# Performance work log

Hardware: AMD Instinct MI355X
Metric: run time of the kernel (lower is better)

The kernel has to match this reference:

```python
import jax, jax.numpy as jnp
import numpy as np

DIM = 1024
N_HEADS = 16
HEAD_DIM = DIM // N_HEADS
SCALE = HEAD_DIM ** (-0.5)


def setup_inputs() -> dict:
    key = jax.random.key(0)
    ks = jax.random.split(key, 5)
    B, N = 2, 2048
    x = jax.random.normal(ks[0], (B, N, DIM), dtype=jnp.float32)
    # torch nn.Linear weight layout: (out_features, in_features)
    qkv_w = jax.random.normal(ks[1], (3 * DIM, DIM), dtype=jnp.float32) * 0.02
    qkv_b = jax.random.normal(ks[2], (3 * DIM,), dtype=jnp.float32) * 0.02
    proj_w = jax.random.normal(ks[3], (DIM, DIM), dtype=jnp.float32) * 0.02
    proj_b = jax.random.normal(ks[4], (DIM,), dtype=jnp.float32) * 0.02
    return {"x": x, "qkv_w": qkv_w, "qkv_b": qkv_b, "proj_w": proj_w, "proj_b": proj_b}


def reference(x, qkv_w, qkv_b, proj_w, proj_b):
    B, N, C = x.shape
    # QKV projection: (B,N,C) -> (B,N,3C)
    qkv = jnp.einsum('bnc,oc->bno', x, qkv_w) + qkv_b
    # (B,N,3,H,Dh) -> (3,B,H,N,Dh)
    qkv = qkv.reshape(B, N, 3, N_HEADS, HEAD_DIM).transpose(2, 0, 3, 1, 4)
    q, k, v = qkv[0], qkv[1], qkv[2]
    attn = jnp.einsum('bhqd,bhkd->bhqk', q, k) * SCALE
    attn = jax.nn.softmax(attn, axis=-1)
    out = jnp.einsum('bhqk,bhkd->bhqd', attn, v)
    out = out.transpose(0, 2, 1, 3).reshape(B, N, C)  # concat heads
    out = jnp.einsum('bnc,oc->bno', out, proj_w) + proj_b
    return out
```

## Files before the change

### kernel.cpp

```cpp
#include <hip/hip_runtime.h>

#define DIM 1024
#define NHEADS 16
#define HD 64
#define NSEQ 2048
#define MROWS 4096
#define QKV_LD 3072

typedef __attribute__((ext_vector_type(8))) short short8;
typedef __attribute__((ext_vector_type(4))) short short4v;
typedef __attribute__((ext_vector_type(4))) float f32x4;

typedef __attribute__((address_space(1))) void gvoid_t;
typedef __attribute__((address_space(3))) void lvoid_t;

#if __has_builtin(__builtin_amdgcn_exp2f)
#define EXP2(x) __builtin_amdgcn_exp2f(x)
#else
#define EXP2(x) exp2f(x)
#endif

#define EXP_SCALE 0.18033688011112042f

#define PHI(r) (((r) & 7) ^ ((((r) >> 3) & 3) << 1))

__device__ __forceinline__ unsigned short f2bf(float f) {
  unsigned int u = __builtin_bit_cast(unsigned int, f);
  u += 0x7FFFu + ((u >> 16) & 1u);
  return (unsigned short)(u >> 16);
}

__device__ __forceinline__ void gl_lds16(const void* g, void* l) {
  __builtin_amdgcn_global_load_lds((gvoid_t*)g, (lvoid_t*)l, 16, 0, 0);
}

__global__ __launch_bounds__(256) void cast_bf16_3(
    const float* __restrict__ x, const float* __restrict__ wq,
    const float* __restrict__ wp,
    unsigned short* __restrict__ xb, unsigned short* __restrict__ wqb,
    unsigned short* __restrict__ wpb)
{
  int g = blockIdx.x * 256 + threadIdx.x;
  const float* src;
  unsigned short* dst;
  if (g < 1048576)            { src = x  + (size_t)g * 4;              dst = xb  + (size_t)g * 4; }
  else if (g < 1048576 + 786432) { int t = g - 1048576; src = wq + (size_t)t * 4; dst = wqb + (size_t)t * 4; }
  else                        { int t = g - 1048576 - 786432; src = wp + (size_t)t * 4; dst = wpb + (size_t)t * 4; }
  float4 v = *(const float4*)src;
  ushort4 o;
  o.x = f2bf(v.x); o.y = f2bf(v.y); o.z = f2bf(v.z); o.w = f2bf(v.w);
  *(ushort4*)dst = o;
}

__global__ __launch_bounds__(256) void gemm_nt(
    const unsigned short* __restrict__ A,
    const unsigned short* __restrict__ Bw,
    const float* __restrict__ bias,
    int K, int mode,
    unsigned short* __restrict__ oq,
    unsigned short* __restrict__ ovt,
    float* __restrict__ of)
{
  __shared__ unsigned short As[128 * 64];
  __shared__ unsigned short Bs[128 * 64];

  const int tid  = threadIdx.x;
  const int wave = tid >> 6, lane = tid & 63;
  const int quad = lane >> 4, l15 = lane & 15;
  const int mblk = blockIdx.x * 128;
  const int nblk = blockIdx.y * 128;
  const int wrow = (wave >> 1) * 64, wcol = (wave & 1) * 64;

  f32x4 acc[4][4] = {};

  const int sr8 = lane >> 3;
  const int sp8 = lane & 7;
  const int qc  = sp8 ^ sr8;
  const unsigned short* aB = A  + (size_t)(mblk + wave * 32 + sr8) * K + qc * 8;
  const unsigned short* bB = Bw + (size_t)(nblk + wave * 32 + sr8) * K + qc * 8;

  for (int k0 = 0; k0 < K; k0 += 64) {
    __syncthreads();
#pragma unroll
    for (int i = 0; i < 4; ++i) {
      gl_lds16(aB + (size_t)(i * 8) * K + k0, As + (wave * 32 + i * 8) * 64);
      gl_lds16(bB + (size_t)(i * 8) * K + k0, Bs + (wave * 32 + i * 8) * 64);
    }
    asm volatile("s_waitcnt vmcnt(0)" ::: "memory");
    __syncthreads();

#pragma unroll
    for (int ks = 0; ks < 2; ++ks) {
      short8 af[4], bf8[4];
#pragma unroll
      for (int mt = 0; mt < 4; ++mt) {
        int row = wrow + mt * 16 + l15;
        af[mt] = *(const short8*)(As + row * 64 + (((ks * 4 + quad) ^ (row & 7)) * 8));
      }
#pragma unroll
      for (int nt = 0; nt < 4; ++nt) {
        int row = wcol + nt * 16 + l15;
        bf8[nt] = *(const short8*)(Bs + row * 64 + (((ks * 4 + quad) ^ (row & 7)) * 8));
      }
#pragma unroll
      for (int mt = 0; mt < 4; ++mt)
#pragma unroll
        for (int nt = 0; nt < 4; ++nt)
          acc[mt][nt] = __builtin_amdgcn_mfma_f32_16x16x32_bf16(af[mt], bf8[nt], acc[mt][nt], 0, 0, 0);
    }
  }

  float bv[4];
#pragma unroll
  for (int nt = 0; nt < 4; ++nt) bv[nt] = bias[nblk + wcol + nt * 16 + l15];

  if (mode == 0) {
#pragma unroll
    for (int mt = 0; mt < 4; ++mt) {
      int row0 = mblk + wrow + mt * 16 + quad * 4;
#pragma unroll
      for (int nt = 0; nt < 4; ++nt) {
        int col = nblk + wcol + nt * 16 + l15;
#pragma unroll
        for (int r = 0; r < 4; ++r)
          of[(size_t)(row0 + r) * DIM + col] = acc[mt][nt][r] + bv[nt];
      }
    }
  } else if (nblk < 2048) {
    const float qs = (nblk < 1024) ? EXP_SCALE : 1.0f;
#pragma unroll
    for (int mt = 0; mt < 4; ++mt) {
      int row0 = mblk + wrow + mt * 16 + quad * 4;
#pragma unroll
      for (int nt = 0; nt < 4; ++nt) {
        int col = nblk + wcol + nt * 16 + l15;
#pragma unroll
        for (int r = 0; r < 4; ++r)
          oq[(size_t)(row0 + r) * QKV_LD + col] = f2bf((acc[mt][nt][r] + bv[nt]) * qs);
      }
    }
  } else {
#pragma unroll
    for (int mt = 0; mt < 4; ++mt) {
      int row0 = mblk + wrow + mt * 16 + quad * 4;
      int n0 = row0 & (NSEQ - 1);
      int bb = row0 >> 11;
      int tt  = n0 >> 6;
      int kin = n0 & 63;
      int g   = kin >> 5;
      int qv2 = (kin >> 3) & 3;
      int j0  = kin & 7;
#pragma unroll
      for (int nt = 0; nt < 4; ++nt) {
        int colr = (nblk - 2048) + wcol + nt * 16 + l15;
        int bh = bb * NHEADS + (colr >> 6);
        int d  = colr & 63;
        int dt = d >> 4, dl15 = d & 15;
        ushort4 pk;
        pk.x = f2bf(acc[mt][nt][0] + bv[nt]);
        pk.y = f2bf(acc[mt][nt][1] + bv[nt]);
        pk.z = f2bf(acc[mt][nt][2] + bv[nt]);
        pk.w = f2bf(acc[mt][nt][3] + bv[nt]);
        size_t off = (size_t)(bh * 32 + tt) * 4096 + g * 2048 + dt * 512
                   + qv2 * 128 + dl15 * 8 + j0;
        *(ushort4*)(ovt + off) = pk;
      }
    }
  }
}

__global__ __launch_bounds__(256) void gemm_nt64(
    const unsigned short* __restrict__ A,
    const unsigned short* __restrict__ Bw,
    const float* __restrict__ bias,
    int K,
    float* __restrict__ of)
{
  __shared__ unsigned short As[64 * 64];
  __shared__ unsigned short Bs[128 * 64];

  const int tid  = threadIdx.x;
  const int wave = tid >> 6, lane = tid & 63;
  const int quad = lane >> 4, l15 = lane & 15;
  const int mblk = blockIdx.x * 64;
  const int nblk = blockIdx.y * 128;
  const int wrow = (wave >> 1) * 32, wcol = (wave & 1) * 64;

  f32x4 acc[2][4] = {};

  const int sr8 = lane >> 3;
  const int sp8 = lane & 7;
  const int qc  = sp8 ^ sr8;
  const unsigned short* aB = A  + (size_t)(mblk + wave * 16 + sr8) * K + qc * 8;
  const unsigned short* bB = Bw + (size_t)(nblk + wave * 32 + sr8) * K + qc * 8;

  for (int k0 = 0; k0 < K; k0 += 64) {
    __syncthreads();
    gl_lds16(aB + k0,                 As + (wave * 16) * 64);
    gl_lds16(aB + (size_t)8 * K + k0, As + (wave * 16 + 8) * 64);
#pragma unroll
    for (int i = 0; i < 4; ++i)
      gl_lds16(bB + (size_t)(i * 8) * K + k0, Bs + (wave * 32 + i * 8) * 64);
    asm volatile("s_waitcnt vmcnt(0)" ::: "memory");
    __syncthreads();

#pragma unroll
    for (int ks = 0; ks < 2; ++ks) {
      short8 af[2], bf8[4];
#pragma unroll
      for (int mt = 0; mt < 2; ++mt) {
        int row = wrow + mt * 16 + l15;
        af[mt] = *(const short8*)(As + row * 64 + (((ks * 4 + quad) ^ (row & 7)) * 8));
      }
#pragma unroll
      for (int nt = 0; nt < 4; ++nt) {
        int row = wcol + nt * 16 + l15;
        bf8[nt] = *(const short8*)(Bs + row * 64 + (((ks * 4 + quad) ^ (row & 7)) * 8));
      }
#pragma unroll
      for (int mt = 0; mt < 2; ++mt)
#pragma unroll
        for (int nt = 0; nt < 4; ++nt)
          acc[mt][nt] = __builtin_amdgcn_mfma_f32_16x16x32_bf16(af[mt], bf8[nt], acc[mt][nt], 0, 0, 0);
    }
  }

  float bv[4];
#pragma unroll
  for (int nt = 0; nt < 4; ++nt) bv[nt] = bias[nblk + wcol + nt * 16 + l15];

#pragma unroll
  for (int mt = 0; mt < 2; ++mt) {
    int row0 = mblk + wrow + mt * 16 + quad * 4;
#pragma unroll
    for (int nt = 0; nt < 4; ++nt) {
      int col = nblk + wcol + nt * 16 + l15;
#pragma unroll
      for (int r = 0; r < 4; ++r)
        of[(size_t)(row0 + r) * DIM + col] = acc[mt][nt][r] + bv[nt];
    }
  }
}

__global__ __launch_bounds__(256, 4) void attn_fused(
    const unsigned short* __restrict__ qkv,
    const unsigned short* __restrict__ vfrag,
    unsigned short* __restrict__ aout)
{
  __shared__ unsigned short Ks[2][64 * 64];
  __shared__ unsigned short Vs[2][64 * 64];

  const int tid  = threadIdx.x;
  const int wave = tid >> 6, lane = tid & 63;
  const int quad = lane >> 4, l15 = lane & 15;
  const int qh = wave & 1;
  const int kh = wave >> 1;
  const int bh = blockIdx.x, b = bh >> 4, h = bh & 15;
  const int q0 = blockIdx.y * 64;
  const size_t qkvB = (size_t)b * NSEQ * QKV_LD;

  short8 qf[2][2];
#pragma unroll
  for (int nq = 0; nq < 2; ++nq)
#pragma unroll
    for (int ks = 0; ks < 2; ++ks)
      qf[nq][ks] = *(const short8*)(qkv + qkvB +
          (size_t)(q0 + qh * 32 + nq * 16 + l15) * QKV_LD + h * HD + ks * 32 + quad * 8);

  f32x4 oacc[4][2] = {};
  float lsum[2] = {0.f, 0.f};

  const int sr8 = lane >> 3;
  const int sp8 = lane & 7;

  const int r0s = wave * 16 + sr8;
  const int r1s = wave * 16 + 8 + sr8;
  const int qc0 = sp8 ^ PHI(r0s);
  const int qc1 = sp8 ^ PHI(r1s);
  const unsigned short* kBase = qkv + qkvB + DIM + h * HD;
  const unsigned short* kSrc0 = kBase + (size_t)r0s * QKV_LD + qc0 * 8;
  const unsigned short* kSrc1 = kBase + (size_t)r1s * QKV_LD + qc1 * 8;
  const unsigned short* vfT = vfrag + (size_t)bh * 32 * 4096 + wave * 512 + lane * 8;

  const int prow0 = kh * 32 + ((l15 & ~3) << 1) + (l15 & 3);
  const int prow1 = prow0 + 4;

  auto stage = [&](int bufi, int kkn) {
    gl_lds16(kSrc0 + (size_t)kkn * QKV_LD, &Ks[bufi][(wave * 16) * 64]);
    gl_lds16(kSrc1 + (size_t)kkn * QKV_LD, &Ks[bufi][(wave * 16 + 8) * 64]);
    const unsigned short* vs = vfT + (size_t)(kkn >> 6) * 4096;
    gl_lds16(vs,        &Vs[bufi][wave * 512]);
    gl_lds16(vs + 2048, &Vs[bufi][wave * 512 + 2048]);
  };

  stage(0, 0);
  asm volatile("s_waitcnt vmcnt(0)" ::: "memory");
  __syncthreads();

  for (int kk = 0; kk < NSEQ; kk += 64) {
    const int cur = (kk >> 6) & 1;
    if (kk + 64 < NSEQ) stage(cur ^ 1, kk + 64);

    const unsigned short* Kc = &Ks[cur][0];
    const unsigned short* Vc = &Vs[cur][0];

    short8 kf[2][2];
#pragma unroll
    for (int ks = 0; ks < 2; ++ks) {
      kf[0][ks] = *(const short8*)(Kc + prow0 * 64 + (((ks * 4 + quad) ^ PHI(prow0)) * 8));
      kf[1][ks] = *(const short8*)(Kc + prow1 * 64 + (((ks * 4 + quad) ^ PHI(prow1)) * 8));
    }

    f32x4 sacc[2][2] = {};
    __builtin_amdgcn_s_setprio(1);
#pragma unroll
    for (int kt = 0; kt < 2; ++kt)
#pragma unroll
      for (int nq = 0; nq < 2; ++nq) {
        sacc[kt][nq] = __builtin_amdgcn_mfma_f32_16x16x32_bf16(kf[kt][0], qf[nq][0], sacc[kt][nq], 0, 0, 0);
        sacc[kt][nq] = __builtin_amdgcn_mfma_f32_16x16x32_bf16(kf[kt][1], qf[nq][1], sacc[kt][nq], 0, 0, 0);
      }
    __builtin_amdgcn_s_setprio(0);

    short8 vf8[4];
#pragma unroll
    for (int dt = 0; dt < 4; ++dt)
      vf8[dt] = *(const short8*)(Vc + kh * 2048 + dt * 512 + lane * 8);

#pragma unroll
    for (int nq = 0; nq < 2; ++nq) {
      float p0 = EXP2(sacc[0][nq][0]);
      float p1 = EXP2(sacc[0][nq][1]);
      float p2 = EXP2(sacc[0][nq][2]);
      float p3 = EXP2(sacc[0][nq][3]);
      float p4 = EXP2(sacc[1][nq][0]);
      float p5 = EXP2(sacc[1][nq][1]);
      float p6 = EXP2(sacc[1][nq][2]);
      float p7 = EXP2(sacc[1][nq][3]);
      lsum[nq] += ((p0 + p1) + (p2 + p3)) + ((p4 + p5) + (p6 + p7));
      unsigned r0 = __builtin_bit_cast(unsigned, p0) + 0x8000u;
      unsigned r1 = __builtin_bit_cast(unsigned, p1) + 0x8000u;
      unsigned r2 = __builtin_bit_cast(unsigned, p2) + 0x8000u;
      unsigned r3 = __builtin_bit_cast(unsigned, p3) + 0x8000u;
      unsigned r4 = __builtin_bit_cast(unsigned, p4) + 0x8000u;
      unsigned r5 = __builtin_bit_cast(unsigned, p5) + 0x8000u;
      unsigned r6 = __builtin_bit_cast(unsigned, p6) + 0x8000u;
      unsigned r7 = __builtin_bit_cast(unsigned, p7) + 0x8000u;
      uint4 pd;
      pd.x = __builtin_amdgcn_perm(r1, r0, 0x07060302u);
      pd.y = __builtin_amdgcn_perm(r3, r2, 0x07060302u);
      pd.z = __builtin_amdgcn_perm(r5, r4, 0x07060302u);
      pd.w = __builtin_amdgcn_perm(r7, r6, 0x07060302u);
      short8 pf = __builtin_bit_cast(short8, pd);
      __builtin_amdgcn_s_setprio(1);
#pragma unroll
      for (int dt = 0; dt < 4; ++dt)
        oacc[dt][nq] = __builtin_amdgcn_mfma_f32_16x16x32_bf16(vf8[dt], pf, oacc[dt][nq], 0, 0, 0);
      __builtin_amdgcn_s_setprio(0);
    }

    asm volatile("s_waitcnt vmcnt(0)" ::: "memory");
    __syncthreads();
  }

#pragma unroll
  for (int nq = 0; nq < 2; ++nq) {
    lsum[nq] += __shfl_xor(lsum[nq], 16);
    lsum[nq] += __shfl_xor(lsum[nq], 32);
  }

  {
    float* red0 = (float*)&Ks[0][0];
    float* red1 = (float*)&Vs[0][0];
    float* red = qh ? red1 : red0;
    const int base = lane * 34;
    if (kh == 1) {
#pragma unroll
      for (int dt = 0; dt < 4; ++dt)
#pragma unroll
        for (int nq = 0; nq < 2; ++nq)
#pragma unroll
          for (int r = 0; r < 4; ++r)
            red[base + dt * 8 + nq * 4 + r] = oacc[dt][nq][r];
      red[base + 32] = lsum[0];
      red[base + 33] = lsum[1];
    }
    __syncthreads();
    if (kh == 0) {
#pragma unroll
      for (int dt = 0; dt < 4; ++dt)
#pragma unroll
        for (int nq = 0; nq < 2; ++nq)
#pragma unroll
          for (int r = 0; r < 4; ++r)
            oacc[dt][nq][r] += red[base + dt * 8 + nq * 4 + r];
      lsum[0] += red[base + 32];
      lsum[1] += red[base + 33];

      const size_t outB = (size_t)(b * NSEQ + q0 + qh * 32) * DIM + h * HD;
#pragma unroll
      for (int nq = 0; nq < 2; ++nq) {
        float inv = 1.0f / lsum[nq];
        const size_t rowB = outB + (size_t)(nq * 16 + l15) * DIM;
#pragma unroll
        for (int dt = 0; dt < 4; ++dt) {
          unsigned a0 = __builtin_bit_cast(unsigned, oacc[dt][nq][0] * inv) + 0x8000u;
          unsigned a1 = __builtin_bit_cast(unsigned, oacc[dt][nq][1] * inv) + 0x8000u;
          unsigned a2 = __builtin_bit_cast(unsigned, oacc[dt][nq][2] * inv) + 0x8000u;
          unsigned a3 = __builtin_bit_cast(unsigned, oacc[dt][nq][3] * inv) + 0x8000u;
          uint2 st;
          st.x = __builtin_amdgcn_perm(a1, a0, 0x07060302u);
          st.y = __builtin_amdgcn_perm(a3, a2, 0x07060302u);
          *(uint2*)(aout + rowB + dt * 16 + quad * 4) = st;
        }
      }
    }
  }
}

extern "C" void kernel_launch(void* const* d_in, const int* in_sizes, int n_in,
                              void* d_out, int out_size, void* d_ws, size_t ws_size,
                              hipStream_t stream) {
  (void)in_sizes; (void)n_in; (void)out_size; (void)ws_size;
  const float* x      = (const float*)d_in[0];
  const float* qkv_w  = (const float*)d_in[1];
  const float* qkv_b  = (const float*)d_in[2];
  const float* proj_w = (const float*)d_in[3];
  const float* proj_b = (const float*)d_in[4];
  float* out = (float*)d_out;

  char* ws = (char*)d_ws;
  unsigned short* xb   = (unsigned short*)(ws);
  unsigned short* wqb  = (unsigned short*)(ws + ( 8u << 20));
  unsigned short* wpb  = (unsigned short*)(ws + (14u << 20));
  unsigned short* qkv  = (unsigned short*)(ws + (16u << 20));
  unsigned short* vtw  = (unsigned short*)(ws + (40u << 20));
  unsigned short* attn = (unsigned short*)(ws + (48u << 20));

  cast_bf16_3<<<8192, 256, 0, stream>>>(x, qkv_w, proj_w, xb, wqb, wpb);
  gemm_nt<<<dim3(32, 24), 256, 0, stream>>>(xb, wqb, qkv_b, DIM, 1, qkv, vtw, nullptr);
  attn_fused<<<dim3(32, 32), 256, 0, stream>>>(qkv, vtw, attn);
  gemm_nt64<<<dim3(64, 8), 256, 0, stream>>>(attn, wpb, proj_b, DIM, out);
}
```

Before: 177.9 us.

## Split attention block across eight waves with one query tile per wave

Doubles the attention block to 512 threads so each wave handles a single 16-row query tile instead of two, halving per-wave MFMA work and register state. K/V staging is spread across eight waves, one 16-byte load each per buffer. The cross-wave reduction layout is adapted to four query quarters. This aims to raise parallelism and latency hiding, but it reloads K/V fragments from LDS for each query tile, which doubles LDS read traffic per block and costs more barrier participants.

```diff
diff --git a/kernel.cpp b/kernel.cpp
--- a/kernel.cpp
+++ b/kernel.cpp
@@ -242,7 +242,7 @@
   }
 }
 
-__global__ __launch_bounds__(256, 4) void attn_fused(
+__global__ __launch_bounds__(512, 8) void attn_fused(
     const unsigned short* __restrict__ qkv,
     const unsigned short* __restrict__ vfrag,
     unsigned short* __restrict__ aout)
@@ -253,45 +253,34 @@
   const int tid  = threadIdx.x;
   const int wave = tid >> 6, lane = tid & 63;
   const int quad = lane >> 4, l15 = lane & 15;
-  const int qh = wave & 1;
-  const int kh = wave >> 1;
+  const int qq = wave & 3;
+  const int kh = wave >> 2;
   const int bh = blockIdx.x, b = bh >> 4, h = bh & 15;
   const int q0 = blockIdx.y * 64;
   const size_t qkvB = (size_t)b * NSEQ * QKV_LD;
 
-  short8 qf[2][2];
-#pragma unroll
-  for (int nq = 0; nq < 2; ++nq)
-#pragma unroll
-    for (int ks = 0; ks < 2; ++ks)
-      qf[nq][ks] = *(const short8*)(qkv + qkvB +
-          (size_t)(q0 + qh * 32 + nq * 16 + l15) * QKV_LD + h * HD + ks * 32 + quad * 8);
-
-  f32x4 oacc[4][2] = {};
-  float lsum[2] = {0.f, 0.f};
-
-  const int sr8 = lane >> 3;
-  const int sp8 = lane & 7;
-
-  const int r0s = wave * 16 + sr8;
-  const int r1s = wave * 16 + 8 + sr8;
-  const int qc0 = sp8 ^ PHI(r0s);
-  const int qc1 = sp8 ^ PHI(r1s);
-  const unsigned short* kBase = qkv + qkvB + DIM + h * HD;
-  const unsigned short* kSrc0 = kBase + (size_t)r0s * QKV_LD + qc0 * 8;
-  const unsigned short* kSrc1 = kBase + (size_t)r1s * QKV_LD + qc1 * 8;
-  const unsigned short* vfT = vfrag + (size_t)bh * 32 * 4096 + wave * 512 + lane * 8;
+  short8 qf[2];
+#pragma unroll
+  for (int ks = 0; ks < 2; ++ks)
+    qf[ks] = *(const short8*)(qkv + qkvB +
+        (size_t)(q0 + qq * 16 + l15) * QKV_LD + h * HD + ks * 32 + quad * 8);
+
+  f32x4 oacc[4] = {};
+  float lsum = 0.f;
+
+  const int krow = tid >> 3;
+  const int sp8  = tid & 7;
+  const int qc   = sp8 ^ PHI(krow);
+  const unsigned short* kSrc = qkv + qkvB + DIM + h * HD + (size_t)krow * QKV_LD + qc * 8;
+  const unsigned short* vSrc = vfrag + (size_t)bh * 32 * 4096 + wave * 512 + lane * 8;
+
+  auto stage = [&](int bufi, int kkn) {
+    gl_lds16(kSrc + (size_t)kkn * QKV_LD,        &Ks[bufi][wave * 512]);
+    gl_lds16(vSrc + (size_t)(kkn >> 6) * 4096,   &Vs[bufi][wave * 512]);
+  };
 
   const int prow0 = kh * 32 + ((l15 & ~3) << 1) + (l15 & 3);
   const int prow1 = prow0 + 4;
-
-  auto stage = [&](int bufi, int kkn) {
-    gl_lds16(kSrc0 + (size_t)kkn * QKV_LD, &Ks[bufi][(wave * 16) * 64]);
-    gl_lds16(kSrc1 + (size_t)kkn * QKV_LD, &Ks[bufi][(wave * 16 + 8) * 64]);
-    const unsigned short* vs = vfT + (size_t)(kkn >> 6) * 4096;
-    gl_lds16(vs,        &Vs[bufi][wave * 512]);
-    gl_lds16(vs + 2048, &Vs[bufi][wave * 512 + 2048]);
-  };
 
   stage(0, 0);
   asm volatile("s_waitcnt vmcnt(0)" ::: "memory");
@@ -311,15 +300,13 @@
       kf[1][ks] = *(const short8*)(Kc + prow1 * 64 + (((ks * 4 + quad) ^ PHI(prow1)) * 8));
     }
 
-    f32x4 sacc[2][2] = {};
+    f32x4 sacc[2] = {};
     __builtin_amdgcn_s_setprio(1);
 #pragma unroll
-    for (int kt = 0; kt < 2; ++kt)
-#pragma unroll
-      for (int nq = 0; nq < 2; ++nq) {
-        sacc[kt][nq] = __builtin_amdgcn_mfma_f32_16x16x32_bf16(kf[kt][0], qf[nq][0], sacc[kt][nq], 0, 0, 0);
-        sacc[kt][nq] = __builtin_amdgcn_mfma_f32_16x16x32_bf16(kf[kt][1], qf[nq][1], sacc[kt][nq], 0, 0, 0);
-      }
+    for (int kt = 0; kt < 2; ++kt) {
+      sacc[kt] = __builtin_amdgcn_mfma_f32_16x16x32_bf16(kf[kt][0], qf[0], sacc[kt], 0, 0, 0);
+      sacc[kt] = __builtin_amdgcn_mfma_f32_16x16x32_bf16(kf[kt][1], qf[1], sacc[kt], 0, 0, 0);
+    }
     __builtin_amdgcn_s_setprio(0);
 
     short8 vf8[4];
@@ -327,17 +314,16 @@
     for (int dt = 0; dt < 4; ++dt)
       vf8[dt] = *(const short8*)(Vc + kh * 2048 + dt * 512 + lane * 8);
 
-#pragma unroll
-    for (int nq = 0; nq < 2; ++nq) {
-      float p0 = EXP2(sacc[0][nq][0]);
-      float p1 = EXP2(sacc[0][nq][1]);
-      float p2 = EXP2(sacc[0][nq][2]);
-      float p3 = EXP2(sacc[0][nq][3]);
-      float p4 = EXP2(sacc[1][nq][0]);
-      float p5 = EXP2(sacc[1][nq][1]);
-      float p6 = EXP2(sacc[1][nq][2]);
-      float p7 = EXP2(sacc[1][nq][3]);
-      lsum[nq] += ((p0 + p1) + (p2 + p3)) + ((p4 + p5) + (p6 + p7));
+    {
+      float p0 = EXP2(sacc[0][0]);
+      float p1 = EXP2(sacc[0][1]);
+      float p2 = EXP2(sacc[0][2]);
+      float p3 = EXP2(sacc[0][3]);
+      float p4 = EXP2(sacc[1][0]);
+      float p5 = EXP2(sacc[1][1]);
+      float p6 = EXP2(sacc[1][2]);
+      float p7 = EXP2(sacc[1][3]);
+      lsum += ((p0 + p1) + (p2 + p3)) + ((p4 + p5) + (p6 + p7));
       unsigned r0 = __builtin_bit_cast(unsigned, p0) + 0x8000u;
       unsigned r1 = __builtin_bit_cast(unsigned, p1) + 0x8000u;
       unsigned r2 = __builtin_bit_cast(unsigned, p2) + 0x8000u;
@@ -355,7 +341,7 @@
       __builtin_amdgcn_s_setprio(1);
 #pragma unroll
       for (int dt = 0; dt < 4; ++dt)
-        oacc[dt][nq] = __builtin_amdgcn_mfma_f32_16x16x32_bf16(vf8[dt], pf, oacc[dt][nq], 0, 0, 0);
+        oacc[dt] = __builtin_amdgcn_mfma_f32_16x16x32_bf16(vf8[dt], pf, oacc[dt], 0, 0, 0);
       __builtin_amdgcn_s_setprio(0);
     }
 
@@ -363,56 +349,41 @@
     __syncthreads();
   }
 
-#pragma unroll
-  for (int nq = 0; nq < 2; ++nq) {
-    lsum[nq] += __shfl_xor(lsum[nq], 16);
-    lsum[nq] += __shfl_xor(lsum[nq], 32);
-  }
+  lsum += __shfl_xor(lsum, 16);
+  lsum += __shfl_xor(lsum, 32);
 
   {
-    float* red0 = (float*)&Ks[0][0];
-    float* red1 = (float*)&Vs[0][0];
-    float* red = qh ? red1 : red0;
-    const int base = lane * 34;
+    float* red = ((qq < 2) ? (float*)&Ks[0][0] : (float*)&Vs[0][0])
+               + ((qq & 1) * 64 + lane) * 18;
     if (kh == 1) {
 #pragma unroll
       for (int dt = 0; dt < 4; ++dt)
 #pragma unroll
-        for (int nq = 0; nq < 2; ++nq)
-#pragma unroll
-          for (int r = 0; r < 4; ++r)
-            red[base + dt * 8 + nq * 4 + r] = oacc[dt][nq][r];
-      red[base + 32] = lsum[0];
-      red[base + 33] = lsum[1];
+        for (int r = 0; r < 4; ++r)
+          red[dt * 4 + r] = oacc[dt][r];
+      red[16] = lsum;
     }
     __syncthreads();
     if (kh == 0) {
 #pragma unroll
       for (int dt = 0; dt < 4; ++dt)
 #pragma unroll
-        for (int nq = 0; nq < 2; ++nq)
-#pragma unroll
-          for (int r = 0; r < 4; ++r)
-            oacc[dt][nq][r] += red[base + dt * 8 + nq * 4 + r];
-      lsum[0] += red[base + 32];
-      lsum[1] += red[base + 33];
-
-      const size_t outB = (size_t)(b * NSEQ + q0 + qh * 32) * DIM + h * HD;
-#pragma unroll
-      for (int nq = 0; nq < 2; ++nq) {
-        float inv = 1.0f / lsum[nq];
-        const size_t rowB = outB + (size_t)(nq * 16 + l15) * DIM;
-#pragma unroll
-        for (int dt = 0; dt < 4; ++dt) {
-          unsigned a0 = __builtin_bit_cast(unsigned, oacc[dt][nq][0] * inv) + 0x8000u;
-          unsigned a1 = __builtin_bit_cast(unsigned, oacc[dt][nq][1] * inv) + 0x8000u;
-          unsigned a2 = __builtin_bit_cast(unsigned, oacc[dt][nq][2] * inv) + 0x8000u;
-          unsigned a3 = __builtin_bit_cast(unsigned, oacc[dt][nq][3] * inv) + 0x8000u;
-          uint2 st;
-          st.x = __builtin_amdgcn_perm(a1, a0, 0x07060302u);
-          st.y = __builtin_amdgcn_perm(a3, a2, 0x07060302u);
-          *(uint2*)(aout + rowB + dt * 16 + quad * 4) = st;
-        }
+        for (int r = 0; r < 4; ++r)
+          oacc[dt][r] += red[dt * 4 + r];
+      lsum += red[16];
+
+      float inv = 1.0f / lsum;
+      const size_t rowB = (size_t)(b * NSEQ + q0 + qq * 16 + l15) * DIM + h * HD;
+#pragma unroll
+      for (int dt = 0; dt < 4; ++dt) {
+        unsigned a0 = __builtin_bit_cast(unsigned, oacc[dt][0] * inv) + 0x8000u;
+        unsigned a1 = __builtin_bit_cast(unsigned, oacc[dt][1] * inv) + 0x8000u;
+        unsigned a2 = __builtin_bit_cast(unsigned, oacc[dt][2] * inv) + 0x8000u;
+        unsigned a3 = __builtin_bit_cast(unsigned, oacc[dt][3] * inv) + 0x8000u;
+        uint2 st;
+        st.x = __builtin_amdgcn_perm(a1, a0, 0x07060302u);
+        st.y = __builtin_amdgcn_perm(a3, a2, 0x07060302u);
+        *(uint2*)(aout + rowB + dt * 16 + quad * 4) = st;
       }
     }
   }
@@ -439,6 +410,6 @@
 
   cast_bf16_3<<<8192, 256, 0, stream>>>(x, qkv_w, proj_w, xb, wqb, wpb);
   gemm_nt<<<dim3(32, 24), 256, 0, stream>>>(xb, wqb, qkv_b, DIM, 1, qkv, vtw, nullptr);
-  attn_fused<<<dim3(32, 32), 256, 0, stream>>>(qkv, vtw, attn);
+  attn_fused<<<dim3(32, 32), 512, 0, stream>>>(qkv, vtw, attn);
   gemm_nt64<<<dim3(64, 8), 256, 0, stream>>>(attn, wpb, proj_b, DIM, out);
 }
```

Result: slower. 195.6 us (+9.9%).

## Double-buffer LDS in GEMM kernels with K-step 32 prefetch

Applied to the files above, without the earlier changes.

Both GEMM kernels now keep two LDS buffers with a K-tile of 32 instead of one buffer of 64. Each iteration starts the direct global-to-LDS loads for the next tile before running MFMAs on the current one, so load latency can hide behind compute. The LDS swizzle is changed to a 4-chunk XOR to fit the narrower rows. The cost is twice as many K iterations, each with a vmcnt wait and barrier, and fewer MFMAs per barrier. The narrower swizzle may also cause more LDS bank conflicts.

```diff
diff --git a/kernel.cpp b/kernel.cpp
--- a/kernel.cpp
+++ b/kernel.cpp
@@ -61,8 +61,8 @@
     unsigned short* __restrict__ ovt,
     float* __restrict__ of)
 {
-  __shared__ unsigned short As[128 * 64];
-  __shared__ unsigned short Bs[128 * 64];
+  __shared__ unsigned short As[2][128 * 32];
+  __shared__ unsigned short Bs[2][128 * 32];
 
   const int tid  = threadIdx.x;
   const int wave = tid >> 6, lane = tid & 63;
@@ -73,41 +73,48 @@
 
   f32x4 acc[4][4] = {};
 
-  const int sr8 = lane >> 3;
-  const int sp8 = lane & 7;
-  const int qc  = sp8 ^ sr8;
-  const unsigned short* aB = A  + (size_t)(mblk + wave * 32 + sr8) * K + qc * 8;
-  const unsigned short* bB = Bw + (size_t)(nblk + wave * 32 + sr8) * K + qc * 8;
-
-  for (int k0 = 0; k0 < K; k0 += 64) {
-    __syncthreads();
-#pragma unroll
-    for (int i = 0; i < 4; ++i) {
-      gl_lds16(aB + (size_t)(i * 8) * K + k0, As + (wave * 32 + i * 8) * 64);
-      gl_lds16(bB + (size_t)(i * 8) * K + k0, Bs + (wave * 32 + i * 8) * 64);
-    }
+  const int sr = lane >> 2;
+  const int sq = (lane & 3) ^ (sr & 3);
+  const unsigned short* aBase = A  + (size_t)(mblk + wave * 32 + sr) * K + sq * 8;
+  const unsigned short* bBase = Bw + (size_t)(nblk + wave * 32 + sr) * K + sq * 8;
+
+  auto stage = [&](int bufi, int k0) {
+    gl_lds16(aBase + k0,          &As[bufi][(wave * 32) * 32]);
+    gl_lds16(aBase + 16 * K + k0, &As[bufi][(wave * 32 + 16) * 32]);
+    gl_lds16(bBase + k0,          &Bs[bufi][(wave * 32) * 32]);
+    gl_lds16(bBase + 16 * K + k0, &Bs[bufi][(wave * 32 + 16) * 32]);
+  };
+
+  stage(0, 0);
+  asm volatile("s_waitcnt vmcnt(0)" ::: "memory");
+  __syncthreads();
+
+  for (int k0 = 0; k0 < K; k0 += 32) {
+    const int cur = (k0 >> 5) & 1;
+    if (k0 + 32 < K) stage(cur ^ 1, k0 + 32);
+
+    const unsigned short* Ac = &As[cur][0];
+    const unsigned short* Bc = &Bs[cur][0];
+
+    short8 af[4], bf8[4];
+#pragma unroll
+    for (int mt = 0; mt < 4; ++mt) {
+      int row = wrow + mt * 16 + l15;
+      af[mt] = *(const short8*)(Ac + row * 32 + ((quad ^ (row & 3)) * 8));
+    }
+#pragma unroll
+    for (int nt = 0; nt < 4; ++nt) {
+      int row = wcol + nt * 16 + l15;
+      bf8[nt] = *(const short8*)(Bc + row * 32 + ((quad ^ (row & 3)) * 8));
+    }
+#pragma unroll
+    for (int mt = 0; mt < 4; ++mt)
+#pragma unroll
+      for (int nt = 0; nt < 4; ++nt)
+        acc[mt][nt] = __builtin_amdgcn_mfma_f32_16x16x32_bf16(af[mt], bf8[nt], acc[mt][nt], 0, 0, 0);
+
     asm volatile("s_waitcnt vmcnt(0)" ::: "memory");
     __syncthreads();
-
-#pragma unroll
-    for (int ks = 0; ks < 2; ++ks) {
-      short8 af[4], bf8[4];
-#pragma unroll
-      for (int mt = 0; mt < 4; ++mt) {
-        int row = wrow + mt * 16 + l15;
-        af[mt] = *(const short8*)(As + row * 64 + (((ks * 4 + quad) ^ (row & 7)) * 8));
-      }
-#pragma unroll
-      for (int nt = 0; nt < 4; ++nt) {
-        int row = wcol + nt * 16 + l15;
-        bf8[nt] = *(const short8*)(Bs + row * 64 + (((ks * 4 + quad) ^ (row & 7)) * 8));
-      }
-#pragma unroll
-      for (int mt = 0; mt < 4; ++mt)
-#pragma unroll
-        for (int nt = 0; nt < 4; ++nt)
-          acc[mt][nt] = __builtin_amdgcn_mfma_f32_16x16x32_bf16(af[mt], bf8[nt], acc[mt][nt], 0, 0, 0);
-    }
   }
 
   float bv[4];
@@ -176,8 +183,8 @@
     int K,
     float* __restrict__ of)
 {
-  __shared__ unsigned short As[64 * 64];
-  __shared__ unsigned short Bs[128 * 64];
+  __shared__ unsigned short As[2][64 * 32];
+  __shared__ unsigned short Bs[2][128 * 32];
 
   const int tid  = threadIdx.x;
   const int wave = tid >> 6, lane = tid & 63;
@@ -188,41 +195,47 @@
 
   f32x4 acc[2][4] = {};
 
-  const int sr8 = lane >> 3;
-  const int sp8 = lane & 7;
-  const int qc  = sp8 ^ sr8;
-  const unsigned short* aB = A  + (size_t)(mblk + wave * 16 + sr8) * K + qc * 8;
-  const unsigned short* bB = Bw + (size_t)(nblk + wave * 32 + sr8) * K + qc * 8;
-
-  for (int k0 = 0; k0 < K; k0 += 64) {
-    __syncthreads();
-    gl_lds16(aB + k0,                 As + (wave * 16) * 64);
-    gl_lds16(aB + (size_t)8 * K + k0, As + (wave * 16 + 8) * 64);
-#pragma unroll
-    for (int i = 0; i < 4; ++i)
-      gl_lds16(bB + (size_t)(i * 8) * K + k0, Bs + (wave * 32 + i * 8) * 64);
+  const int sr = lane >> 2;
+  const int sq = (lane & 3) ^ (sr & 3);
+  const unsigned short* aBase = A  + (size_t)(mblk + wave * 16 + sr) * K + sq * 8;
+  const unsigned short* bBase = Bw + (size_t)(nblk + wave * 32 + sr) * K + sq * 8;
+
+  auto stage = [&](int bufi, int k0) {
+    gl_lds16(aBase + k0,          &As[bufi][(wave * 16) * 32]);
+    gl_lds16(bBase + k0,          &Bs[bufi][(wave * 32) * 32]);
+    gl_lds16(bBase + 16 * K + k0, &Bs[bufi][(wave * 32 + 16) * 32]);
+  };
+
+  stage(0, 0);
+  asm volatile("s_waitcnt vmcnt(0)" ::: "memory");
+  __syncthreads();
+
+  for (int k0 = 0; k0 < K; k0 += 32) {
+    const int cur = (k0 >> 5) & 1;
+    if (k0 + 32 < K) stage(cur ^ 1, k0 + 32);
+
+    const unsigned short* Ac = &As[cur][0];
+    const unsigned short* Bc = &Bs[cur][0];
+
+    short8 af[2], bf8[4];
+#pragma unroll
+    for (int mt = 0; mt < 2; ++mt) {
+      int row = wrow + mt * 16 + l15;
+      af[mt] = *(const short8*)(Ac + row * 32 + ((quad ^ (row & 3)) * 8));
+    }
+#pragma unroll
+    for (int nt = 0; nt < 4; ++nt) {
+      int row = wcol + nt * 16 + l15;
+      bf8[nt] = *(const short8*)(Bc + row * 32 + ((quad ^ (row & 3)) * 8));
+    }
+#pragma unroll
+    for (int mt = 0; mt < 2; ++mt)
+#pragma unroll
+      for (int nt = 0; nt < 4; ++nt)
+        acc[mt][nt] = __builtin_amdgcn_mfma_f32_16x16x32_bf16(af[mt], bf8[nt], acc[mt][nt], 0, 0, 0);
+
     asm volatile("s_waitcnt vmcnt(0)" ::: "memory");
     __syncthreads();
-
-#pragma unroll
-    for (int ks = 0; ks < 2; ++ks) {
-      short8 af[2], bf8[4];
-#pragma unroll
-      for (int mt = 0; mt < 2; ++mt) {
-        int row = wrow + mt * 16 + l15;
-        af[mt] = *(const short8*)(As + row * 64 + (((ks * 4 + quad) ^ (row & 7)) * 8));
-      }
-#pragma unroll
-      for (int nt = 0; nt < 4; ++nt) {
-        int row = wcol + nt * 16 + l15;
-        bf8[nt] = *(const short8*)(Bs + row * 64 + (((ks * 4 + quad) ^ (row & 7)) * 8));
-      }
-#pragma unroll
-      for (int mt = 0; mt < 2; ++mt)
-#pragma unroll
-        for (int nt = 0; nt < 4; ++nt)
-          acc[mt][nt] = __builtin_amdgcn_mfma_f32_16x16x32_bf16(af[mt], bf8[nt], acc[mt][nt], 0, 0, 0);
-    }
   }
 
   float bv[4];
```

New measurement: 181.0 us. About the same (+1.7%).
